# Performance work log

Hardware: AMD Instinct MI355X
Metric: run time of the kernel (lower is better)

Reference implementation:

```python
import math
import jax, jax.numpy as jnp
import numpy as np

NUM_HEADS = 16
SIZE = 1024
HEAD = SIZE // NUM_HEADS
MAX_SEQ = 2048
B, L = 4, 1024


def setup_inputs() -> dict:
    key = jax.random.key(0)
    ks = jax.random.split(key, 12)
    s = 1.0 / math.sqrt(SIZE)
    return {
        "k": jax.random.normal(ks[0], (B, L, SIZE), jnp.float32),
        "v": jax.random.normal(ks[1], (B, L, SIZE), jnp.float32),
        "q": jax.random.normal(ks[2], (B, L, SIZE), jnp.float32),
        "mask": jnp.ones((B, 1, L), dtype=bool),
        "E": jax.random.normal(ks[3], (MAX_SEQ, HEAD), jnp.float32),
        "Wk": jax.random.normal(ks[4], (SIZE, SIZE), jnp.float32) * s,
        "bk": jnp.zeros((SIZE,), jnp.float32),
        "Wv": jax.random.normal(ks[5], (SIZE, SIZE), jnp.float32) * s,
        "bv": jnp.zeros((SIZE,), jnp.float32),
        "Wq": jax.random.normal(ks[6], (SIZE, SIZE), jnp.float32) * s,
        "bq": jnp.zeros((SIZE,), jnp.float32),
        "Wo": jax.random.normal(ks[7], (SIZE, SIZE), jnp.float32) * s,
        "bo": jnp.zeros((SIZE,), jnp.float32),
    }


def _attention(k, v, q, mask, E, Wk, bk, Wv, bv, Wq, bq, Wo, bo):
    b, lk, d = k.shape
    lq = q.shape[1]
    hd = E.shape[1]
    h = d // hd
    # project and split heads -> [b, h, len, hd]
    kh = (k @ Wk + bk).reshape(b, lk, h, hd).transpose(0, 2, 1, 3)
    vh = (v @ Wv + bv).reshape(b, lk, h, hd).transpose(0, 2, 1, 3)
    qh = (q @ Wq + bq).reshape(b, lq, h, hd).transpose(0, 2, 1, 3)

    scores = jnp.einsum("bhqd,bhkd->bhqk", qh, kh)  # [b,h,lq,lk]

    # relative position bias (Music-Transformer skewing)
    e = E[E.shape[0] - lq:, :]                       # [lq, hd]
    QE = jnp.einsum("bhld,md->bhlm", qh, e)          # [b,h,lq,lq]
    tri = (jnp.arange(lq)[None, :] <= jnp.arange(lq)[:, None]).astype(QE.dtype)
    QE = QE * tri                                    # qe masking
    padded = jnp.pad(QE, ((0, 0), (0, 0), (0, 0), (1, 0)))  # pad left of last dim
    Srel = padded.reshape(b, h, lq + 1, lq)[:, :, 1:, :]      # [b,h,lq,lq]
    if lk > lq:
        Srel = jnp.pad(Srel, ((0, 0), (0, 0), (0, 0), (0, lk - lq)))
    elif lk < lq:
        Srel = Srel[:, :, :, :lk]
    scores = scores + Srel

    scores = scores / math.sqrt(hd)
    scores = jnp.where(mask[:, None], scores, -jnp.inf)  # mask [b,1,lk] -> [b,1,1,lk]
    attn = jax.nn.softmax(scores, axis=-1)
    ctx = jnp.einsum("bhqk,bhkd->bhqd", attn, vh)
    ctx = ctx.transpose(0, 2, 1, 3).reshape(b, lq, h * hd)
    return ctx @ Wo + bo


def reference(k, v, q, mask, E, Wk, bk, Wv, bv, Wq, bq, Wo, bo):
    return _attention(k, v, q, mask, E, Wk, bk, Wv, bv, Wq, bq, Wo, bo)
```

## Files before the change

### kernel.cpp

```cpp
#include <hip/hip_runtime.h>
#include <stdint.h>

typedef unsigned short u16;
typedef __attribute__((ext_vector_type(8))) short short8;
typedef __attribute__((ext_vector_type(4))) float f32x4;
typedef __attribute__((ext_vector_type(4))) unsigned short u16x4;

#define MFMA16(a, b, c) __builtin_amdgcn_mfma_f32_16x16x32_bf16((a), (b), (c), 0, 0, 0)

__device__ __forceinline__ float bf2f(u16 u) {
    union { uint32_t i; float f; } v;
    v.i = ((uint32_t)u) << 16;
    return v.f;
}
__device__ __forceinline__ u16 f2bf(float f) {
    union { float f; uint32_t i; } v;
    v.f = f;
    uint32_t r = v.i + 0x7FFF + ((v.i >> 16) & 1);
    return (u16)(r >> 16);
}
__device__ __forceinline__ float scrub(float x) {
    union { float f; uint32_t i; } v;
    v.f = x;
    return ((v.i & 0x7F800000u) == 0x7F800000u) ? 0.f : x;
}

__global__ __launch_bounds__(256) void transpose4(
    const float* __restrict__ W0, const float* __restrict__ W1,
    const float* __restrict__ W2, const float* __restrict__ W3,
    u16* __restrict__ out)
{
    __shared__ u16 t[32][33];
    int z = blockIdx.z;
    const float* W = (z == 0) ? W0 : (z == 1) ? W1 : (z == 2) ? W2 : W3;
    u16* o = out + (size_t)z * 1048576;
    int tx = threadIdx.x & 31, ty = threadIdx.x >> 5;
    int x = blockIdx.x * 32 + tx;
    int yb = blockIdx.y * 32;
#pragma unroll
    for (int j = 0; j < 4; j++)
        t[ty + j * 8][tx] = f2bf(W[(size_t)(yb + ty + j * 8) * 1024 + x]);
    __syncthreads();
    int xo = yb + tx;
    int yob = blockIdx.x * 32;
#pragma unroll
    for (int j = 0; j < 4; j++)
        o[(size_t)(yob + ty + j * 8) * 1024 + xo] = t[tx][ty + j * 8];
}

__global__ __launch_bounds__(256) void ecvt(
    const float* __restrict__ e, u16* __restrict__ eb)
{
    int i = (blockIdx.x * 256 + threadIdx.x) * 4;
    f32x4 v = *(const f32x4*)&e[i];
    u16x4 o;
#pragma unroll
    for (int r = 0; r < 4; r++) o[r] = f2bf(v[r]);
    *(u16x4*)&eb[i] = o;
}

__global__ __launch_bounds__(256) void cvt3(
    const float* __restrict__ a0, const float* __restrict__ a1,
    const float* __restrict__ a2, u16* __restrict__ o0,
    u16* __restrict__ o1, u16* __restrict__ o2)
{
    int z = blockIdx.y;
    const float* a = (z == 0) ? a0 : (z == 1) ? a1 : a2;
    u16* o = (z == 0) ? o0 : (z == 1) ? o1 : o2;
    int i = (blockIdx.x * 256 + threadIdx.x) * 4;
    f32x4 v = *(const f32x4*)&a[i];
    u16x4 p;
#pragma unroll
    for (int r = 0; r < 4; r++) p[r] = f2bf(v[r]);
    *(u16x4*)&o[i] = p;
}

__global__ __launch_bounds__(256) void gemm_qkv(
    const u16* __restrict__ A0, const u16* __restrict__ A1,
    const u16* __restrict__ A2, const u16* __restrict__ Wt,
    const float* __restrict__ bi0, const float* __restrict__ bi1,
    const float* __restrict__ bi2, u16* __restrict__ khp,
    u16* __restrict__ vhtp, u16* __restrict__ qhp)
{
    __shared__ u16 As[128][40];
    __shared__ u16 Bs[128][40];
    const int K = 1024;
    int z = blockIdx.z;
    const u16* A = (z == 0) ? A0 : (z == 1) ? A1 : A2;
    const float* bias = (z == 0) ? bi0 : (z == 1) ? bi1 : bi2;
    const u16* Bt = Wt + (size_t)z * 1048576;
    u16* outb = (z == 0) ? khp : (z == 1) ? vhtp : qhp;

    int n0 = blockIdx.x * 128, m0 = blockIdx.y * 128;
    int tid = threadIdx.x;
    int w = tid >> 6, lane = tid & 63, g = lane >> 4, cc = lane & 15;
    int wm = (w >> 1) * 64, wn = (w & 1) * 64;
    int tr = tid >> 2, tc = (tid & 3) * 8;

    f32x4 acc[4][4];
#pragma unroll
    for (int i = 0; i < 4; i++)
#pragma unroll
        for (int j = 0; j < 4; j++) acc[i][j] = (f32x4){0.f, 0.f, 0.f, 0.f};

    for (int kb = 0; kb < K; kb += 32) {
        short8 a0 = *(const short8*)&A[(size_t)(m0 + tr) * K + kb + tc];
        short8 a1 = *(const short8*)&A[(size_t)(m0 + 64 + tr) * K + kb + tc];
        short8 b0 = *(const short8*)&Bt[(size_t)(n0 + tr) * K + kb + tc];
        short8 b1 = *(const short8*)&Bt[(size_t)(n0 + 64 + tr) * K + kb + tc];
        __syncthreads();
        *(short8*)&As[tr][tc] = a0;
        *(short8*)&As[64 + tr][tc] = a1;
        *(short8*)&Bs[tr][tc] = b0;
        *(short8*)&Bs[64 + tr][tc] = b1;
        __syncthreads();
        short8 af[4], bf[4];
#pragma unroll
        for (int mt = 0; mt < 4; mt++) af[mt] = *(const short8*)&As[wm + mt * 16 + cc][g * 8];
#pragma unroll
        for (int nt = 0; nt < 4; nt++) bf[nt] = *(const short8*)&Bs[wn + nt * 16 + cc][g * 8];
#pragma unroll
        for (int mt = 0; mt < 4; mt++)
#pragma unroll
            for (int nt = 0; nt < 4; nt++)
                acc[mt][nt] = MFMA16(af[mt], bf[nt], acc[mt][nt]);
    }

#pragma unroll
    for (int mt = 0; mt < 4; mt++) {
        int rl = wm + mt * 16 + g * 4;
#pragma unroll
        for (int nt = 0; nt < 4; nt++) {
            int n = n0 + wn + nt * 16 + cc;
            float bb = bias[n];
            if (z == 1) {
                int m = m0 + rl;
                int b_ = m >> 10, l_ = m & 1023, h_ = n >> 6, d_ = n & 63;
                u16x4 pk;
#pragma unroll
                for (int r = 0; r < 4; r++) pk[r] = f2bf(scrub(acc[mt][nt][r] + bb));
                *(u16x4*)&outb[((size_t)(b_ * 16 + h_) * 64 + d_) * 1024 + l_] = pk;
            } else {
#pragma unroll
                for (int r = 0; r < 4; r++) {
                    int m = m0 + rl + r;
                    int b_ = m >> 10, l_ = m & 1023, h_ = n >> 6, d_ = n & 63;
                    outb[((size_t)(b_ * 16 + h_) * 1024 + l_) * 64 + d_] =
                        f2bf(scrub(acc[mt][nt][r] + bb));
                }
            }
        }
    }
}

__global__ __launch_bounds__(256) void gemm_out(
    const u16* __restrict__ A, const u16* __restrict__ Bt,
    const float* __restrict__ bias, float* __restrict__ outf)
{
    __shared__ u16 As[64][40];
    __shared__ u16 Bs[128][40];
    const int K = 1024;
    int n0 = blockIdx.x * 128, m0 = blockIdx.y * 64;
    int tid = threadIdx.x;
    int w = tid >> 6, lane = tid & 63, g = lane >> 4, cc = lane & 15;
    int wm = (w >> 1) * 32, wn = (w & 1) * 64;
    int tr = tid >> 2, tc = (tid & 3) * 8;

    f32x4 acc[2][4];
#pragma unroll
    for (int i = 0; i < 2; i++)
#pragma unroll
        for (int j = 0; j < 4; j++) acc[i][j] = (f32x4){0.f, 0.f, 0.f, 0.f};

    for (int kb = 0; kb < K; kb += 32) {
        short8 a0 = *(const short8*)&A[(size_t)(m0 + tr) * K + kb + tc];
        short8 b0 = *(const short8*)&Bt[(size_t)(n0 + tr) * K + kb + tc];
        short8 b1 = *(const short8*)&Bt[(size_t)(n0 + 64 + tr) * K + kb + tc];
        __syncthreads();
        if (tr < 64) *(short8*)&As[tr][tc] = a0;
        *(short8*)&Bs[tr][tc] = b0;
        *(short8*)&Bs[64 + tr][tc] = b1;
        __syncthreads();
        short8 af[2], bf[4];
#pragma unroll
        for (int mt = 0; mt < 2; mt++) af[mt] = *(const short8*)&As[wm + mt * 16 + cc][g * 8];
#pragma unroll
        for (int nt = 0; nt < 4; nt++) bf[nt] = *(const short8*)&Bs[wn + nt * 16 + cc][g * 8];
#pragma unroll
        for (int mt = 0; mt < 2; mt++)
#pragma unroll
            for (int nt = 0; nt < 4; nt++)
                acc[mt][nt] = MFMA16(af[mt], bf[nt], acc[mt][nt]);
    }

#pragma unroll
    for (int mt = 0; mt < 2; mt++) {
        int rl = wm + mt * 16 + g * 4;
#pragma unroll
        for (int nt = 0; nt < 4; nt++) {
            int n = n0 + wn + nt * 16 + cc;
            float bb = bias[n];
#pragma unroll
            for (int r = 0; r < 4; r++)
                outf[(size_t)(m0 + rl + r) * 1024 + n] = scrub(acc[mt][nt][r] + bb);
        }
    }
}

__global__ __launch_bounds__(256) void srel_gemm(
    const u16* __restrict__ qh, const u16* __restrict__ eb, u16* __restrict__ Sp)
{
    __shared__ u16 As[128][40];
    __shared__ u16 Bs[128][40];
    int mb = blockIdx.x * 128;
    int qb = blockIdx.y * 128;
    int bh = blockIdx.z;
    const u16* A = qh + (size_t)bh * 65536;
    u16* O = Sp + (size_t)bh * 1048576;
    int tid = threadIdx.x;
    int w = tid >> 6, lane = tid & 63, g = lane >> 4, cc = lane & 15;
    int wm = (w >> 1) * 64, wn = (w & 1) * 64;

    if (mb == 0 && tid < 128) {
        int j = qb + tid;
        if (j < 1023) O[(size_t)j * 1024 + j + 1] = 0;
    }

    if (mb > qb + 284 && mb + qb < 769) return;

    f32x4 acc[4][4];
#pragma unroll
    for (int i = 0; i < 4; i++)
#pragma unroll
        for (int j = 0; j < 4; j++) acc[i][j] = (f32x4){0.f, 0.f, 0.f, 0.f};

    if (mb <= qb + 127) {
        int tr = tid >> 2, tc = (tid & 3) * 8;
#pragma unroll
        for (int kb = 0; kb < 64; kb += 32) {
            short8 a0 = *(const short8*)&A[(size_t)(qb + tr) * 64 + kb + tc];
            short8 a1 = *(const short8*)&A[(size_t)(qb + 64 + tr) * 64 + kb + tc];
            short8 b0 = *(const short8*)&eb[(size_t)(mb + tr) * 64 + kb + tc];
            short8 b1 = *(const short8*)&eb[(size_t)(mb + 64 + tr) * 64 + kb + tc];
            __syncthreads();
            *(short8*)&As[tr][tc] = a0;
            *(short8*)&As[64 + tr][tc] = a1;
            *(short8*)&Bs[tr][tc] = b0;
            *(short8*)&Bs[64 + tr][tc] = b1;
            __syncthreads();
            short8 af[4], bf[4];
#pragma unroll
            for (int mt = 0; mt < 4; mt++) af[mt] = *(const short8*)&As[wm + mt * 16 + cc][g * 8];
#pragma unroll
            for (int nt = 0; nt < 4; nt++) bf[nt] = *(const short8*)&Bs[wn + nt * 16 + cc][g * 8];
#pragma unroll
            for (int mt = 0; mt < 4; mt++)
#pragma unroll
                for (int nt = 0; nt < 4; nt++)
                    acc[mt][nt] = MFMA16(af[mt], bf[nt], acc[mt][nt]);
        }
    }

#pragma unroll
    for (int mt = 0; mt < 4; mt++)
#pragma unroll
        for (int nt = 0; nt < 4; nt++)
#pragma unroll
            for (int r = 0; r < 4; r++) {
                int j = qb + wm + mt * 16 + g * 4 + r;
                int c = mb + wn + nt * 16 + cc;
                u16 v = (c <= j) ? f2bf(scrub(acc[mt][nt][r])) : (u16)0;
                if (c >= 1023 - j)
                    O[(size_t)j * 1024 + (c + j - 1023)] = v;
                else if (j > 0 && c <= j + 157)
                    O[(size_t)(j - 1) * 1024 + (c + j + 1)] = v;
            }
}

__global__ __launch_bounds__(256) void flash(
    const u16* __restrict__ qh, const u16* __restrict__ kh,
    const u16* __restrict__ vht, const u16* __restrict__ Sp,
    u16* __restrict__ ctx)
{
    __shared__ u16 Plds[4][16][136];
    int qt = blockIdx.x, bh = blockIdx.y;
    int w = threadIdx.x >> 6, lane = threadIdx.x & 63, g = lane >> 4, cc = lane & 15;
    const u16* Q = qh + (size_t)bh * 65536;
    const u16* Kp = kh + (size_t)bh * 65536;
    const u16* Vp = vht + (size_t)bh * 65536;
    const u16* Sb = Sp + (size_t)bh * 1048576;
    int q0 = qt * 64 + w * 16;
    int row = g * 4;

    short8 qf[2];
#pragma unroll
    for (int ks = 0; ks < 2; ks++)
        qf[ks] = *(const short8*)&Q[(size_t)(q0 + cc) * 64 + ks * 32 + g * 8];

    float mi[4], li[4];
    f32x4 O[4];
#pragma unroll
    for (int r = 0; r < 4; r++) { mi[r] = -1e30f; li[r] = 0.f; }
#pragma unroll
    for (int d = 0; d < 4; d++) O[d] = (f32x4){0.f, 0.f, 0.f, 0.f};

    const float LOG2E = 1.44269504088896f;
    int qw1 = q0 + 15;

    short8 bnd[4];
    bool needCur = (2 * qw1 >= 1023) || (q0 <= 125);
    if (needCur) {
#pragma unroll
        for (int r = 0; r < 4; r++)
            bnd[r] = *(const short8*)&Sb[(size_t)(q0 + row + r) * 1024 + cc * 8];
    }

    for (int kt = 0; kt < 8; kt++) {
        int k0 = kt * 128;

        f32x4 sc[8];
#pragma unroll
        for (int nt = 0; nt < 8; nt++) sc[nt] = (f32x4){0.f, 0.f, 0.f, 0.f};
#pragma unroll
        for (int nt = 0; nt < 8; nt++) {
            const u16* kr = &Kp[(size_t)(k0 + cc * 8 + nt) * 64 + g * 8];
            short8 b0 = *(const short8*)&kr[0];
            short8 b1 = *(const short8*)&kr[32];
            sc[nt] = MFMA16(qf[0], b0, sc[nt]);
            sc[nt] = MFMA16(qf[1], b1, sc[nt]);
        }

        if (needCur) {
#pragma unroll
            for (int r = 0; r < 4; r++)
#pragma unroll
                for (int nt = 0; nt < 8; nt++)
                    sc[nt][r] += bf2f((u16)bnd[r][nt]);
        }

        bool needNxt = false;
        if (kt < 7) {
            int k0n = k0 + 128;
            needNxt = (k0n <= 2 * qw1 - 1023) ||
                      ((k0n + 127 >= q0 + 2) && (k0n <= 2 * qw1 + 3));
            if (needNxt) {
#pragma unroll
                for (int r = 0; r < 4; r++)
                    bnd[r] = *(const short8*)&Sb[(size_t)(q0 + row + r) * 1024 + k0n + cc * 8];
            }
        }
        needCur = needNxt;

#pragma unroll
        for (int nt = 0; nt < 8; nt++)
#pragma unroll
            for (int r = 0; r < 4; r++) sc[nt][r] *= 0.125f;

#pragma unroll
        for (int r = 0; r < 4; r++) {
            float mx = sc[0][r];
#pragma unroll
            for (int nt = 1; nt < 8; nt++) mx = fmaxf(mx, sc[nt][r]);
            mx = fmaxf(mx, __shfl_xor(mx, 1));
            mx = fmaxf(mx, __shfl_xor(mx, 2));
            mx = fmaxf(mx, __shfl_xor(mx, 4));
            mx = fmaxf(mx, __shfl_xor(mx, 8));
            float mnew = fmaxf(mi[r], mx);
            float alpha = exp2f((mi[r] - mnew) * LOG2E);
            mi[r] = mnew;
            float rs = 0.f;
#pragma unroll
            for (int nt = 0; nt < 8; nt++) {
                float p = exp2f((sc[nt][r] - mnew) * LOG2E);
                sc[nt][r] = p;
                rs += p;
            }
            rs += __shfl_xor(rs, 1);
            rs += __shfl_xor(rs, 2);
            rs += __shfl_xor(rs, 4);
            rs += __shfl_xor(rs, 8);
            li[r] = li[r] * alpha + rs;
#pragma unroll
            for (int d = 0; d < 4; d++) O[d][r] *= alpha;
        }

#pragma unroll
        for (int r = 0; r < 4; r++) {
            short8 pk;
#pragma unroll
            for (int nt = 0; nt < 8; nt++) pk[nt] = (short)f2bf(sc[nt][r]);
            *(short8*)&Plds[w][row + r][cc * 8] = pk;
        }

#pragma unroll
        for (int ks = 0; ks < 4; ks++) {
            short8 a = *(const short8*)&Plds[w][cc][ks * 32 + g * 8];
#pragma unroll
            for (int d = 0; d < 4; d++) {
                short8 vb = *(const short8*)&Vp[(size_t)(d * 16 + cc) * 1024 + k0 + ks * 32 + g * 8];
                O[d] = MFMA16(a, vb, O[d]);
            }
        }
    }

    int b_ = bh >> 4, h_ = bh & 15;
#pragma unroll
    for (int d = 0; d < 4; d++)
#pragma unroll
        for (int r = 0; r < 4; r++) {
            int l_ = q0 + row + r;
            ctx[((size_t)b_ * 1024 + l_) * 1024 + h_ * 64 + d * 16 + cc] =
                f2bf(O[d][r] / li[r]);
        }
}

extern "C" void kernel_launch(void* const* d_in, const int* in_sizes, int n_in,
                              void* d_out, int out_size, void* d_ws, size_t ws_size,
                              hipStream_t stream)
{
    const float *k_in = nullptr, *v_in = nullptr, *q_in = nullptr, *E = nullptr;
    const float* W[4] = {nullptr, nullptr, nullptr, nullptr};
    const float* bs[4] = {nullptr, nullptr, nullptr, nullptr};
    int nqkv = 0, nW = 0, nb = 0;
    for (int i = 0; i < n_in; i++) {
        int s = in_sizes[i];
        const float* p = (const float*)d_in[i];
        if (s == 4194304) {
            if (nqkv == 0) k_in = p; else if (nqkv == 1) v_in = p; else if (nqkv == 2) q_in = p;
            nqkv++;
        } else if (s == 131072) {
            E = p;
        } else if (s == 1048576) {
            if (nW < 4) W[nW] = p;
            nW++;
        } else if (s == 1024) {
            if (nb < 4) bs[nb] = p;
            nb++;
        }
    }

    char* ws = (char*)d_ws;
    u16* Wt   = (u16*)ws;
    u16* khp  = (u16*)(ws + (8u << 20));
    u16* vhtp = (u16*)(ws + (16u << 20));
    u16* qhp  = (u16*)(ws + (24u << 20));
    u16* ctxp = (u16*)(ws + (32u << 20));
    u16* eb   = (u16*)(ws + (40u << 20));
    u16* kb   = (u16*)(ws + (48u << 20));
    u16* vb   = (u16*)(ws + (56u << 20));
    u16* qb   = (u16*)(ws + (64u << 20));
    u16* Sp   = (u16*)(ws + (48u << 20));

    const size_t M1 = 1048576;
    transpose4<<<dim3(32, 32, 4), 256, 0, stream>>>(W[0], W[1], W[2], W[3], Wt);
    ecvt<<<dim3(64), 256, 0, stream>>>(E + 65536, eb);
    cvt3<<<dim3(4096, 3), 256, 0, stream>>>(k_in, v_in, q_in, kb, vb, qb);
    gemm_qkv<<<dim3(8, 32, 3), 256, 0, stream>>>(kb, vb, qb, Wt,
                                                 bs[0], bs[1], bs[2],
                                                 khp, vhtp, qhp);
    srel_gemm<<<dim3(8, 8, 64), 256, 0, stream>>>(qhp, eb, Sp);
    flash<<<dim3(16, 64), 256, 0, stream>>>(qhp, khp, vhtp, Sp, ctxp);
    gemm_out<<<dim3(8, 64), 256, 0, stream>>>(ctxp, Wt + 3 * M1, bs[3], (float*)d_out);
}
```

Baseline: 436.1 us.

## Split flash attention KV range across two wave groups and merge in LDS

The flash kernel now launches 512 threads per block. Two groups of four waves each process half of the key tiles for the same 64 query rows. The second group writes its partial max, sum and output accumulators to shared memory, and the first group merges them with rescaling before writing ctx. This doubles the waves working on each query tile and halves the serial KV loop length per wave. The cost is extra LDS (about 34 KB more), a block barrier, and fewer resident blocks per CU because of the larger block size.

New measurement: 420.0 us. 3.7% less time.

```diff
diff --git a/kernel.cpp b/kernel.cpp
--- a/kernel.cpp
+++ b/kernel.cpp
@@ -277,19 +277,23 @@
             }
 }
 
-__global__ __launch_bounds__(256) void flash(
+__global__ __launch_bounds__(512) void flash(
     const u16* __restrict__ qh, const u16* __restrict__ kh,
     const u16* __restrict__ vht, const u16* __restrict__ Sp,
     u16* __restrict__ ctx)
 {
-    __shared__ u16 Plds[4][16][136];
+    __shared__ u16 Plds[8][16][136];
+    __shared__ float OM[4][16][64];
+    __shared__ float ML[4][16][2];
     int qt = blockIdx.x, bh = blockIdx.y;
-    int w = threadIdx.x >> 6, lane = threadIdx.x & 63, g = lane >> 4, cc = lane & 15;
+    int tid = threadIdx.x;
+    int w = tid >> 6, lane = tid & 63, g = lane >> 4, cc = lane & 15;
+    int half = w >> 2, wq = w & 3;
     const u16* Q = qh + (size_t)bh * 65536;
     const u16* Kp = kh + (size_t)bh * 65536;
     const u16* Vp = vht + (size_t)bh * 65536;
     const u16* Sb = Sp + (size_t)bh * 1048576;
-    int q0 = qt * 64 + w * 16;
+    int q0 = qt * 64 + wq * 16;
     int row = g * 4;
 
     short8 qf[2];
@@ -306,16 +310,19 @@
 
     const float LOG2E = 1.44269504088896f;
     int qw1 = q0 + 15;
+    int ktBeg = half * 4, ktEnd = ktBeg + 4;
 
     short8 bnd[4];
-    bool needCur = (2 * qw1 >= 1023) || (q0 <= 125);
+    int k0s = ktBeg * 128;
+    bool needCur = (k0s <= 2 * qw1 - 1023) ||
+                   ((k0s + 127 >= q0 + 2) && (k0s <= 2 * qw1 + 3));
     if (needCur) {
 #pragma unroll
         for (int r = 0; r < 4; r++)
-            bnd[r] = *(const short8*)&Sb[(size_t)(q0 + row + r) * 1024 + cc * 8];
-    }
-
-    for (int kt = 0; kt < 8; kt++) {
+            bnd[r] = *(const short8*)&Sb[(size_t)(q0 + row + r) * 1024 + k0s + cc * 8];
+    }
+
+    for (int kt = ktBeg; kt < ktEnd; kt++) {
         int k0 = kt * 128;
 
         f32x4 sc[8];
@@ -339,7 +346,7 @@
         }
 
         bool needNxt = false;
-        if (kt < 7) {
+        if (kt < ktEnd - 1) {
             int k0n = k0 + 128;
             needNxt = (k0n <= 2 * qw1 - 1023) ||
                       ((k0n + 127 >= q0 + 2) && (k0n <= 2 * qw1 + 3));
@@ -403,15 +410,37 @@
         }
     }
 
-    int b_ = bh >> 4, h_ = bh & 15;
-#pragma unroll
-    for (int d = 0; d < 4; d++)
+    if (half == 1) {
 #pragma unroll
         for (int r = 0; r < 4; r++) {
+            ML[wq][row + r][0] = mi[r];
+            ML[wq][row + r][1] = li[r];
+#pragma unroll
+            for (int d = 0; d < 4; d++)
+                OM[wq][row + r][d * 16 + cc] = O[d][r];
+        }
+    }
+    __syncthreads();
+
+    if (half == 0) {
+        int b_ = bh >> 4, h_ = bh & 15;
+#pragma unroll
+        for (int r = 0; r < 4; r++) {
+            float m2 = ML[wq][row + r][0];
+            float l2 = ML[wq][row + r][1];
+            float mn = fmaxf(mi[r], m2);
+            float a1 = exp2f((mi[r] - mn) * LOG2E);
+            float a2 = exp2f((m2 - mn) * LOG2E);
+            float ln = li[r] * a1 + l2 * a2;
             int l_ = q0 + row + r;
-            ctx[((size_t)b_ * 1024 + l_) * 1024 + h_ * 64 + d * 16 + cc] =
-                f2bf(O[d][r] / li[r]);
-        }
+#pragma unroll
+            for (int d = 0; d < 4; d++) {
+                float o = O[d][r] * a1 + OM[wq][row + r][d * 16 + cc] * a2;
+                ctx[((size_t)b_ * 1024 + l_) * 1024 + h_ * 64 + d * 16 + cc] =
+                    f2bf(o / ln);
+            }
+        }
+    }
 }
 
 extern "C" void kernel_launch(void* const* d_in, const int* in_sizes, int n_in,
@@ -459,6 +488,6 @@
                                                  bs[0], bs[1], bs[2],
                                                  khp, vhtp, qhp);
     srel_gemm<<<dim3(8, 8, 64), 256, 0, stream>>>(qhp, eb, Sp);
-    flash<<<dim3(16, 64), 256, 0, stream>>>(qhp, khp, vhtp, Sp, ctxp);
+    flash<<<dim3(16, 64), 512, 0, stream>>>(qhp, khp, vhtp, Sp, ctxp);
     gemm_out<<<dim3(8, 64), 256, 0, stream>>>(ctxp, Wt + 3 * M1, bs[3], (float*)d_out);
 }
```
